# Performance work log

Hardware: AMD Instinct MI355X
Metric: run time of the kernel (lower is better)

## Reference

```python
import jax, jax.numpy as jnp
import numpy as np

N = 16384          # points in the (single-batch) cloud
K = 16             # boundary_k
C = 20             # num semantic classes (ScanNet-style)
IGNORE = -1        # ignore_index
BOUNDARY_W = 1.0   # boundary_loss_weight


def setup_inputs() -> dict:
    key = jax.random.key(0)
    k1, k2, k3 = jax.random.split(key, 3)
    coord = jax.random.normal(k1, (N, 3), jnp.float32)
    seg_logits = jax.random.normal(k2, (N, C), jnp.float32)
    segment = jax.random.randint(k3, (N,), 0, C, dtype=jnp.int32)
    return {"coord": coord, "seg_logits": seg_logits, "segment": segment, "offset": N}


def _knn_idx(coord):
    # brute-force kNN (loop=False): exclude self via +inf diagonal
    d2 = jnp.sum(coord * coord, axis=1)                       # [N]
    dist = d2[:, None] + d2[None, :] - 2.0 * (coord @ coord.T)  # [N, N]
    dist = dist + jnp.where(jnp.eye(dist.shape[0], dtype=bool), jnp.inf, 0.0)
    _, idx = jax.lax.top_k(-dist, K)                          # [N, K] neighbor (src) indices per center (dst)
    return idx


def _masked_ce(logp_tgt, mask):
    # mean cross-entropy over masked points (matches torch reduction='mean' w/ ignore_index)
    cnt = jnp.sum(mask)
    s = jnp.sum(jnp.where(mask, logp_tgt, 0.0))
    return jnp.where(cnt > 0, -s / jnp.maximum(cnt, 1).astype(logp_tgt.dtype), 0.0)


def reference(coord, seg_logits, segment, offset):
    # --- boundary mask: knn_graph -> per-edge label diff -> scatter-max to dst ---
    nbr = _knn_idx(coord)                                     # [N, K] src indices, dst = row index
    nbr_seg = segment[nbr]                                    # gather: [N, K]
    valid_pt = segment != IGNORE                              # [N]
    valid = (nbr_seg != IGNORE) & valid_pt[:, None]           # per-edge valid
    diff = valid & (nbr_seg != segment[:, None])              # per-edge label mismatch
    boundary = jnp.any(diff, axis=1)                          # scatter-max over dst == row-wise any

    # --- main loss: cross-entropy with ignore_index ---
    logp = jax.nn.log_softmax(seg_logits, axis=-1)            # [N, C]
    tgt = jnp.clip(segment, 0, C - 1)
    logp_tgt = jnp.take_along_axis(logp, tgt[:, None], axis=1)[:, 0]  # [N]
    main_loss = _masked_ce(logp_tgt, valid_pt)

    # --- boundary loss: CE restricted to boundary points (0 if none) ---
    bmask = boundary & valid_pt
    boundary_loss = _masked_ce(logp_tgt, bmask)

    loss = main_loss + BOUNDARY_W * boundary_loss
    return loss
```

## Files before the change

kernel.cpp:

```cpp
#include <hip/hip_runtime.h>
#include <hip/hip_bf16.h>
#include <math.h>

#define N_PTS 16384
#define KNN   16
#define NCLS  20
#define BND_W 1.0f

#define THREADS 512
#define WAVES   8
#define FR      4
#define RPW     (16 * FR)
#define RPB     (WAVES * RPW)
#define RBLKS   (N_PTS / RPB)
#define CPB     512
#define CSPLIT  (N_PTS / CPB)

typedef short  short8 __attribute__((ext_vector_type(8)));
typedef float  f32x4  __attribute__((ext_vector_type(4)));

__device__ __forceinline__ unsigned enc_f(float f) {
    unsigned b = __float_as_uint(f);
    return (b & 0x80000000u) ? ~b : (b | 0x80000000u);
}
__device__ __forceinline__ float dec_f(unsigned u) {
    unsigned b = (u & 0x80000000u) ? (u ^ 0x80000000u) : ~u;
    return __uint_as_float(b);
}

__device__ __forceinline__ unsigned short f2bf(float x) {
    union { __hip_bfloat16 h; unsigned short u; } cv;
    cv.h = __float2bfloat16(x);
    return cv.u;
}
__device__ __forceinline__ float bf2f(unsigned short b) {
    union { __hip_bfloat16 h; unsigned short u; } cv;
    cv.u = b;
    return __bfloat162float(cv.h);
}

__device__ __forceinline__ void build_b(const float* __restrict__ coord,
                                        const int* __restrict__ seg, int j,
                                        unsigned short* out) {
    float x = coord[3 * j], y = coord[3 * j + 1], z = coord[3 * j + 2];
    int lab = seg[j];
    unsigned short xh = f2bf(x), yh = f2bf(y), zh = f2bf(z);
    unsigned short xl = f2bf(x - bf2f(xh));
    unsigned short yl = f2bf(y - bf2f(yh));
    unsigned short zl = f2bf(z - bf2f(zh));
    float h = 0.5f * fmaf(x, x, fmaf(y, y, z * z));
    unsigned short hh = f2bf(h);
    unsigned short hl = f2bf(h - bf2f(hh));
    out[0] = xh; out[1] = xh; out[2] = xl;
    out[3] = yh; out[4] = yh; out[5] = yl;
    out[6] = zh; out[7] = zh; out[8] = zl;
    out[9]  = hh ^ 0x8000u;
    out[10] = hl ^ 0x8000u;
#pragma unroll
    for (int s = 0; s < NCLS; s++) out[11 + s] = (lab == s) ? 0x3F80u : 0u;
    out[31] = (lab < 0) ? 0x3F80u : 0u;
}

template<bool PASS1>
__device__ __forceinline__ void build_a(const float* __restrict__ coord,
                                        const int* __restrict__ seg, int i,
                                        unsigned short* out) {
    float x = coord[3 * i], y = coord[3 * i + 1], z = coord[3 * i + 2];
    int lab = seg[i];
    unsigned short xh = f2bf(x), yh = f2bf(y), zh = f2bf(z);
    unsigned short xl = f2bf(x - bf2f(xh));
    unsigned short yl = f2bf(y - bf2f(yh));
    unsigned short zl = f2bf(z - bf2f(zh));
    out[0] = xh; out[1] = xl; out[2] = xh;
    out[3] = yh; out[4] = yl; out[5] = yh;
    out[6] = zh; out[7] = zl; out[8] = zh;
    out[9] = 0x3F80u; out[10] = 0x3F80u;
    const unsigned short nb = 0xC480u;
#pragma unroll
    for (int s = 0; s < NCLS; s++) out[11 + s] = (PASS1 && lab == s) ? nb : 0u;
    out[31] = PASS1 ? nb : 0u;
}

__global__ __launch_bounds__(256) void k_init(unsigned* __restrict__ smax_enc,
                                              int* __restrict__ cnt,
                                              float* __restrict__ accum,
                                              unsigned* __restrict__ done) {
    int i = blockIdx.x * 256 + threadIdx.x;
    smax_enc[i] = enc_f(-3.0e38f);
    cnt[i] = 0;
    if (i < 4) accum[i] = 0.f;
    if (i == 4) *done = 0u;
}

template<bool PASS1>
__global__ __launch_bounds__(THREADS) void k_pass(const float* __restrict__ coord,
                                                  const int* __restrict__ seg,
                                                  unsigned* __restrict__ smax_enc,
                                                  int* __restrict__ cnt) {
    __shared__ __align__(16) unsigned short smem[CPB * 32];
    const int tid  = threadIdx.x;
    const int lane = tid & 63, wave = tid >> 6;
    const int l15  = lane & 15, l4 = lane >> 4;
    const int rb   = blockIdx.x * RPB;
    const int cb   = blockIdx.y * CPB;

    float thr[FR][4];
    int   cv[FR][4];
    f32x4 rmax[FR];
    if (PASS1) {
#pragma unroll
        for (int f = 0; f < FR; f++)
#pragma unroll
            for (int r = 0; r < 4; r++) rmax[f][r] = -3.0e38f;
    } else {
#pragma unroll
        for (int f = 0; f < FR; f++) {
            int row0 = rb + wave * RPW + f * 16 + l4 * 4;
#pragma unroll
            for (int r = 0; r < 4; r++) {
                thr[f][r] = dec_f(smax_enc[row0 + r]);
                cv[f][r] = 0;
            }
        }
    }

    build_a<PASS1>(coord, seg, rb + tid, &smem[tid * 32]);
    __syncthreads();
    short8 af[FR];
    {
        const short8* ap = (const short8*)smem;
#pragma unroll
        for (int f = 0; f < FR; f++)
            af[f] = ap[(wave * RPW + f * 16 + l15) * 4 + l4];
    }
    __syncthreads();

    {
        __attribute__((aligned(16))) unsigned short be[32];
        build_b(coord, seg, cb + tid, be);
        short8* wp = (short8*)smem;
        int swz = (tid >> 1) & 3;
#pragma unroll
        for (int kb = 0; kb < 4; kb++)
            wp[tid * 4 + (kb ^ swz)] = ((const short8*)be)[kb];
    }
    __syncthreads();

    const short8* bp = (const short8*)smem;
    const int bidx = l15 * 4 + (l4 ^ ((l15 >> 1) & 3));
    const f32x4 zero = {0.f, 0.f, 0.f, 0.f};

#pragma unroll 2
    for (int c0 = 0; c0 < CPB; c0 += 32) {
        short8 bA = bp[bidx + c0 * 4];
        short8 bB = bp[bidx + (c0 + 16) * 4];
        f32x4 dA[FR], dB[FR];
#pragma unroll
        for (int f = 0; f < FR; f++)
            dA[f] = __builtin_amdgcn_mfma_f32_16x16x32_bf16(af[f], bA, zero, 0, 0, 0);
#pragma unroll
        for (int f = 0; f < FR; f++)
            dB[f] = __builtin_amdgcn_mfma_f32_16x16x32_bf16(af[f], bB, zero, 0, 0, 0);
        if (PASS1) {
#pragma unroll
            for (int f = 0; f < FR; f++)
#pragma unroll
                for (int r = 0; r < 4; r++)
                    rmax[f][r] = fmaxf(fmaxf(rmax[f][r], dA[f][r]), dB[f][r]);
        } else {
#pragma unroll
            for (int f = 0; f < FR; f++)
#pragma unroll
                for (int r = 0; r < 4; r++)
                    cv[f][r] += ((dA[f][r] > thr[f][r]) ? 1 : 0)
                              + ((dB[f][r] > thr[f][r]) ? 1 : 0);
        }
    }

    if (PASS1) {
#pragma unroll
        for (int m = 1; m < 16; m <<= 1)
#pragma unroll
            for (int f = 0; f < FR; f++)
#pragma unroll
                for (int r = 0; r < 4; r++)
                    rmax[f][r] = fmaxf(rmax[f][r], __shfl_xor(rmax[f][r], m, 64));
        if (l15 == 0) {
#pragma unroll
            for (int f = 0; f < FR; f++) {
                int row0 = rb + wave * RPW + f * 16 + l4 * 4;
#pragma unroll
                for (int r = 0; r < 4; r++)
                    atomicMax(&smax_enc[row0 + r], enc_f(rmax[f][r]));
            }
        }
    } else {
#pragma unroll
        for (int m = 1; m < 16; m <<= 1)
#pragma unroll
            for (int f = 0; f < FR; f++)
#pragma unroll
                for (int r = 0; r < 4; r++)
                    cv[f][r] += __shfl_xor(cv[f][r], m, 64);
        if (l15 == 0) {
#pragma unroll
            for (int f = 0; f < FR; f++) {
                int row0 = rb + wave * RPW + f * 16 + l4 * 4;
#pragma unroll
                for (int r = 0; r < 4; r++)
                    atomicAdd(&cnt[row0 + r], cv[f][r]);
            }
        }
    }
}

__device__ __forceinline__ float waveReduceSum(float v) {
#pragma unroll
    for (int off = 32; off > 0; off >>= 1) v += __shfl_down(v, off, 64);
    return v;
}

__global__ __launch_bounds__(256) void k_ce(const float* __restrict__ logits,
                                            const int* __restrict__ seg,
                                            const int* __restrict__ cnt,
                                            float* __restrict__ accum,
                                            unsigned* __restrict__ done,
                                            float* __restrict__ out) {
    const int i = blockIdx.x * 256 + threadIdx.x;
    float s_main = 0.f, n_main = 0.f, s_bnd = 0.f, n_bnd = 0.f;
    {
        int s = seg[i];
        bool valid = (s != -1);
        const float4* row4 = (const float4*)(logits + (size_t)i * NCLS);
        float a[NCLS];
        float4 v0 = row4[0], v1 = row4[1], v2 = row4[2], v3 = row4[3], v4 = row4[4];
        a[0]=v0.x; a[1]=v0.y; a[2]=v0.z; a[3]=v0.w;
        a[4]=v1.x; a[5]=v1.y; a[6]=v1.z; a[7]=v1.w;
        a[8]=v2.x; a[9]=v2.y; a[10]=v2.z; a[11]=v2.w;
        a[12]=v3.x; a[13]=v3.y; a[14]=v3.z; a[15]=v3.w;
        a[16]=v4.x; a[17]=v4.y; a[18]=v4.z; a[19]=v4.w;
        float m = a[0];
#pragma unroll
        for (int c = 1; c < NCLS; c++) m = fmaxf(m, a[c]);
        float se = 0.f;
#pragma unroll
        for (int c = 0; c < NCLS; c++) se += __expf(a[c] - m);
        int tgt = min(max(s, 0), NCLS - 1);
        float at = 0.f;
#pragma unroll
        for (int c = 0; c < NCLS; c++) at += (c == tgt) ? a[c] : 0.f;
        float logp = at - m - __logf(se);
        bool bnd = valid && ((cnt[i] - 1) < KNN);
        if (valid) { s_main = logp; n_main = 1.f; }
        if (bnd)   { s_bnd  = logp; n_bnd  = 1.f; }
    }
    s_main = waveReduceSum(s_main);
    n_main = waveReduceSum(n_main);
    s_bnd  = waveReduceSum(s_bnd);
    n_bnd  = waveReduceSum(n_bnd);
    if ((threadIdx.x & 63) == 0) {
        atomicAdd(&accum[0], s_main);
        atomicAdd(&accum[1], n_main);
        atomicAdd(&accum[2], s_bnd);
        atomicAdd(&accum[3], n_bnd);
    }
    __syncthreads();
    if (threadIdx.x == 0) {
        __threadfence();
        unsigned old = atomicAdd(done, 1u);
        if (old == gridDim.x - 1) {
            float sm = atomicAdd(&accum[0], 0.f);
            float cm = atomicAdd(&accum[1], 0.f);
            float sb = atomicAdd(&accum[2], 0.f);
            float cb = atomicAdd(&accum[3], 0.f);
            float main_loss = (cm > 0.f) ? (-sm / fmaxf(cm, 1.f)) : 0.f;
            float bnd_loss  = (cb > 0.f) ? (-sb / fmaxf(cb, 1.f)) : 0.f;
            out[0] = main_loss + BND_W * bnd_loss;
        }
    }
}

extern "C" void kernel_launch(void* const* d_in, const int* in_sizes, int n_in,
                              void* d_out, int out_size, void* d_ws, size_t ws_size,
                              hipStream_t stream) {
    const float* coord  = (const float*)d_in[0];
    const float* logits = (const float*)d_in[1];
    const int*   seg    = (const int*)d_in[2];
    (void)in_sizes; (void)n_in; (void)out_size; (void)ws_size;

    unsigned* smax_enc = (unsigned*)d_ws;
    int*      cnt      = (int*)((char*)d_ws + N_PTS * 4);
    float*    accum    = (float*)((char*)d_ws + 2 * N_PTS * 4);
    unsigned* done     = (unsigned*)((char*)d_ws + 2 * N_PTS * 4 + 16);

    dim3 grid(RBLKS, CSPLIT);
    k_init       <<<N_PTS / 256, 256, 0, stream>>>(smax_enc, cnt, accum, done);
    k_pass<true> <<<grid, THREADS, 0, stream>>>(coord, seg, smax_enc, cnt);
    k_pass<false><<<grid, THREADS, 0, stream>>>(coord, seg, smax_enc, cnt);
    k_ce         <<<N_PTS / 256, 256, 0, stream>>>(logits, seg, cnt, accum, done, (float*)d_out);
}
```

Baseline: 71.98 us.

## Replace atomics with per-split partial buffers and loop over candidate chunks

Each block now handles 256 rows against 1024 candidates, looping over two LDS chunks of 512, with 16 column splits instead of 32. The global atomicMax/atomicAdd reductions are replaced by plain writes into per-split partial arrays, which pass 2 and the CE kernel reduce. This removes the init kernel and the atomic contention. The cost is smaller per-wave row tiles (2 fragments instead of 4, so less B-operand reuse) and extra partial reads in the consumer kernels.

```diff
diff --git a/kernel.cpp b/kernel.cpp
--- a/kernel.cpp
+++ b/kernel.cpp
@@ -9,24 +9,16 @@
 
 #define THREADS 512
 #define WAVES   8
-#define FR      4
-#define RPW     (16 * FR)
+#define RPW     32
 #define RPB     (WAVES * RPW)
 #define RBLKS   (N_PTS / RPB)
-#define CPB     512
-#define CSPLIT  (N_PTS / CPB)
+#define CSPLIT  16
+#define CAND_PB (N_PTS / CSPLIT)
+#define CHUNK   512
+#define NCHUNK  (CAND_PB / CHUNK)
 
 typedef short  short8 __attribute__((ext_vector_type(8)));
 typedef float  f32x4  __attribute__((ext_vector_type(4)));
-
-__device__ __forceinline__ unsigned enc_f(float f) {
-    unsigned b = __float_as_uint(f);
-    return (b & 0x80000000u) ? ~b : (b | 0x80000000u);
-}
-__device__ __forceinline__ float dec_f(unsigned u) {
-    unsigned b = (u & 0x80000000u) ? (u ^ 0x80000000u) : ~u;
-    return __uint_as_float(b);
-}
 
 __device__ __forceinline__ unsigned short f2bf(float x) {
     union { __hip_bfloat16 h; unsigned short u; } cv;
@@ -81,134 +73,132 @@
     out[31] = PASS1 ? nb : 0u;
 }
 
-__global__ __launch_bounds__(256) void k_init(unsigned* __restrict__ smax_enc,
-                                              int* __restrict__ cnt,
-                                              float* __restrict__ accum,
-                                              unsigned* __restrict__ done) {
-    int i = blockIdx.x * 256 + threadIdx.x;
-    smax_enc[i] = enc_f(-3.0e38f);
-    cnt[i] = 0;
-    if (i < 4) accum[i] = 0.f;
-    if (i == 4) *done = 0u;
-}
-
 template<bool PASS1>
-__global__ __launch_bounds__(THREADS) void k_pass(const float* __restrict__ coord,
-                                                  const int* __restrict__ seg,
-                                                  unsigned* __restrict__ smax_enc,
-                                                  int* __restrict__ cnt) {
-    __shared__ __align__(16) unsigned short smem[CPB * 32];
+__global__ __launch_bounds__(THREADS, 6) void k_pass(const float* __restrict__ coord,
+                                                     const int* __restrict__ seg,
+                                                     float* __restrict__ smax_part,
+                                                     int* __restrict__ cnt_part,
+                                                     float* __restrict__ accum,
+                                                     unsigned* __restrict__ done) {
+    __shared__ __align__(16) unsigned short smem[CHUNK * 32];
+    __shared__ float thr_lds[RPB];
     const int tid  = threadIdx.x;
     const int lane = tid & 63, wave = tid >> 6;
     const int l15  = lane & 15, l4 = lane >> 4;
     const int rb   = blockIdx.x * RPB;
-    const int cb   = blockIdx.y * CPB;
-
-    float thr[FR][4];
-    int   cv[FR][4];
-    f32x4 rmax[FR];
-    if (PASS1) {
-#pragma unroll
-        for (int f = 0; f < FR; f++)
-#pragma unroll
-            for (int r = 0; r < 4; r++) rmax[f][r] = -3.0e38f;
-    } else {
-#pragma unroll
-        for (int f = 0; f < FR; f++) {
-            int row0 = rb + wave * RPW + f * 16 + l4 * 4;
-#pragma unroll
-            for (int r = 0; r < 4; r++) {
-                thr[f][r] = dec_f(smax_enc[row0 + r]);
-                cv[f][r] = 0;
-            }
-        }
-    }
-
-    build_a<PASS1>(coord, seg, rb + tid, &smem[tid * 32]);
+    const int split = blockIdx.y;
+    const int cb   = split * CAND_PB;
+
+    if (PASS1 && blockIdx.x == 0 && split == 0 && tid == 0) {
+        accum[0] = 0.f; accum[1] = 0.f; accum[2] = 0.f; accum[3] = 0.f;
+        *done = 0u;
+    }
+
+    if (!PASS1 && tid < RPB) {
+        int row = rb + tid;
+        float m = smax_part[row];
+#pragma unroll
+        for (int s = 1; s < CSPLIT; s++) m = fmaxf(m, smax_part[s * N_PTS + row]);
+        thr_lds[tid] = m;
+    }
+
+    if (tid < RPB) build_a<PASS1>(coord, seg, rb + tid, &smem[tid * 32]);
     __syncthreads();
-    short8 af[FR];
+    short8 af0, af1;
     {
         const short8* ap = (const short8*)smem;
-#pragma unroll
-        for (int f = 0; f < FR; f++)
-            af[f] = ap[(wave * RPW + f * 16 + l15) * 4 + l4];
+        int r0 = wave * RPW + l15;
+        af0 = ap[r0 * 4 + l4];
+        af1 = ap[(r0 + 16) * 4 + l4];
+    }
+    float thr0[4], thr1[4];
+    if (!PASS1) {
+#pragma unroll
+        for (int r = 0; r < 4; r++) {
+            thr0[r] = thr_lds[wave * RPW + l4 * 4 + r];
+            thr1[r] = thr_lds[wave * RPW + 16 + l4 * 4 + r];
+        }
     }
     __syncthreads();
 
-    {
-        __attribute__((aligned(16))) unsigned short be[32];
-        build_b(coord, seg, cb + tid, be);
-        short8* wp = (short8*)smem;
-        int swz = (tid >> 1) & 3;
-#pragma unroll
-        for (int kb = 0; kb < 4; kb++)
-            wp[tid * 4 + (kb ^ swz)] = ((const short8*)be)[kb];
-    }
-    __syncthreads();
+    f32x4 rmax0, rmax1;
+    int cv0[4], cv1[4];
+#pragma unroll
+    for (int r = 0; r < 4; r++) {
+        rmax0[r] = -3.0e38f; rmax1[r] = -3.0e38f;
+        cv0[r] = 0; cv1[r] = 0;
+    }
 
     const short8* bp = (const short8*)smem;
     const int bidx = l15 * 4 + (l4 ^ ((l15 >> 1) & 3));
     const f32x4 zero = {0.f, 0.f, 0.f, 0.f};
 
-#pragma unroll 2
-    for (int c0 = 0; c0 < CPB; c0 += 32) {
-        short8 bA = bp[bidx + c0 * 4];
-        short8 bB = bp[bidx + (c0 + 16) * 4];
-        f32x4 dA[FR], dB[FR];
-#pragma unroll
-        for (int f = 0; f < FR; f++)
-            dA[f] = __builtin_amdgcn_mfma_f32_16x16x32_bf16(af[f], bA, zero, 0, 0, 0);
-#pragma unroll
-        for (int f = 0; f < FR; f++)
-            dB[f] = __builtin_amdgcn_mfma_f32_16x16x32_bf16(af[f], bB, zero, 0, 0, 0);
-        if (PASS1) {
-#pragma unroll
-            for (int f = 0; f < FR; f++)
-#pragma unroll
-                for (int r = 0; r < 4; r++)
-                    rmax[f][r] = fmaxf(fmaxf(rmax[f][r], dA[f][r]), dB[f][r]);
-        } else {
-#pragma unroll
-            for (int f = 0; f < FR; f++)
-#pragma unroll
-                for (int r = 0; r < 4; r++)
-                    cv[f][r] += ((dA[f][r] > thr[f][r]) ? 1 : 0)
-                              + ((dB[f][r] > thr[f][r]) ? 1 : 0);
-        }
-    }
-
+    for (int cc = 0; cc < NCHUNK; cc++) {
+        {
+            __attribute__((aligned(16))) unsigned short be[32];
+            build_b(coord, seg, cb + cc * CHUNK + tid, be);
+            short8* wp = (short8*)smem;
+            int swz = (tid >> 1) & 3;
+#pragma unroll
+            for (int kb = 0; kb < 4; kb++)
+                wp[tid * 4 + (kb ^ swz)] = ((const short8*)be)[kb];
+        }
+        __syncthreads();
+
+#pragma unroll 4
+        for (int c0 = 0; c0 < CHUNK; c0 += 32) {
+            short8 bA = bp[bidx + c0 * 4];
+            short8 bB = bp[bidx + (c0 + 16) * 4];
+            f32x4 dA0 = __builtin_amdgcn_mfma_f32_16x16x32_bf16(af0, bA, zero, 0, 0, 0);
+            f32x4 dA1 = __builtin_amdgcn_mfma_f32_16x16x32_bf16(af1, bA, zero, 0, 0, 0);
+            f32x4 dB0 = __builtin_amdgcn_mfma_f32_16x16x32_bf16(af0, bB, zero, 0, 0, 0);
+            f32x4 dB1 = __builtin_amdgcn_mfma_f32_16x16x32_bf16(af1, bB, zero, 0, 0, 0);
+            if (PASS1) {
+#pragma unroll
+                for (int r = 0; r < 4; r++) {
+                    rmax0[r] = fmaxf(fmaxf(rmax0[r], dA0[r]), dB0[r]);
+                    rmax1[r] = fmaxf(fmaxf(rmax1[r], dA1[r]), dB1[r]);
+                }
+            } else {
+#pragma unroll
+                for (int r = 0; r < 4; r++) {
+                    cv0[r] += ((dA0[r] > thr0[r]) ? 1 : 0) + ((dB0[r] > thr0[r]) ? 1 : 0);
+                    cv1[r] += ((dA1[r] > thr1[r]) ? 1 : 0) + ((dB1[r] > thr1[r]) ? 1 : 0);
+                }
+            }
+        }
+        __syncthreads();
+    }
+
+    const int row0 = rb + wave * RPW + l4 * 4;
     if (PASS1) {
 #pragma unroll
         for (int m = 1; m < 16; m <<= 1)
 #pragma unroll
-            for (int f = 0; f < FR; f++)
-#pragma unroll
-                for (int r = 0; r < 4; r++)
-                    rmax[f][r] = fmaxf(rmax[f][r], __shfl_xor(rmax[f][r], m, 64));
+            for (int r = 0; r < 4; r++) {
+                rmax0[r] = fmaxf(rmax0[r], __shfl_xor(rmax0[r], m, 64));
+                rmax1[r] = fmaxf(rmax1[r], __shfl_xor(rmax1[r], m, 64));
+            }
         if (l15 == 0) {
 #pragma unroll
-            for (int f = 0; f < FR; f++) {
-                int row0 = rb + wave * RPW + f * 16 + l4 * 4;
-#pragma unroll
-                for (int r = 0; r < 4; r++)
-                    atomicMax(&smax_enc[row0 + r], enc_f(rmax[f][r]));
+            for (int r = 0; r < 4; r++) {
+                smax_part[split * N_PTS + row0 + r]      = rmax0[r];
+                smax_part[split * N_PTS + row0 + 16 + r] = rmax1[r];
             }
         }
     } else {
 #pragma unroll
         for (int m = 1; m < 16; m <<= 1)
 #pragma unroll
-            for (int f = 0; f < FR; f++)
-#pragma unroll
-                for (int r = 0; r < 4; r++)
-                    cv[f][r] += __shfl_xor(cv[f][r], m, 64);
+            for (int r = 0; r < 4; r++) {
+                cv0[r] += __shfl_xor(cv0[r], m, 64);
+                cv1[r] += __shfl_xor(cv1[r], m, 64);
+            }
         if (l15 == 0) {
 #pragma unroll
-            for (int f = 0; f < FR; f++) {
-                int row0 = rb + wave * RPW + f * 16 + l4 * 4;
-#pragma unroll
-                for (int r = 0; r < 4; r++)
-                    atomicAdd(&cnt[row0 + r], cv[f][r]);
+            for (int r = 0; r < 4; r++) {
+                cnt_part[split * N_PTS + row0 + r]      = cv0[r];
+                cnt_part[split * N_PTS + row0 + 16 + r] = cv1[r];
             }
         }
     }
@@ -222,7 +212,7 @@
 
 __global__ __launch_bounds__(256) void k_ce(const float* __restrict__ logits,
                                             const int* __restrict__ seg,
-                                            const int* __restrict__ cnt,
+                                            const int* __restrict__ cnt_part,
                                             float* __restrict__ accum,
                                             unsigned* __restrict__ done,
                                             float* __restrict__ out) {
@@ -250,7 +240,10 @@
 #pragma unroll
         for (int c = 0; c < NCLS; c++) at += (c == tgt) ? a[c] : 0.f;
         float logp = at - m - __logf(se);
-        bool bnd = valid && ((cnt[i] - 1) < KNN);
+        int cnt = 0;
+#pragma unroll
+        for (int sp = 0; sp < CSPLIT; sp++) cnt += cnt_part[sp * N_PTS + i];
+        bool bnd = valid && ((cnt - 1) < KNN);
         if (valid) { s_main = logp; n_main = 1.f; }
         if (bnd)   { s_bnd  = logp; n_bnd  = 1.f; }
     }
@@ -288,14 +281,13 @@
     const int*   seg    = (const int*)d_in[2];
     (void)in_sizes; (void)n_in; (void)out_size; (void)ws_size;
 
-    unsigned* smax_enc = (unsigned*)d_ws;
-    int*      cnt      = (int*)((char*)d_ws + N_PTS * 4);
-    float*    accum    = (float*)((char*)d_ws + 2 * N_PTS * 4);
-    unsigned* done     = (unsigned*)((char*)d_ws + 2 * N_PTS * 4 + 16);
+    float*    smax_part = (float*)d_ws;
+    int*      cnt_part  = (int*)((char*)d_ws + CSPLIT * N_PTS * 4);
+    float*    accum     = (float*)((char*)d_ws + 2 * CSPLIT * N_PTS * 4);
+    unsigned* done      = (unsigned*)((char*)d_ws + 2 * CSPLIT * N_PTS * 4 + 16);
 
     dim3 grid(RBLKS, CSPLIT);
-    k_init       <<<N_PTS / 256, 256, 0, stream>>>(smax_enc, cnt, accum, done);
-    k_pass<true> <<<grid, THREADS, 0, stream>>>(coord, seg, smax_enc, cnt);
-    k_pass<false><<<grid, THREADS, 0, stream>>>(coord, seg, smax_enc, cnt);
-    k_ce         <<<N_PTS / 256, 256, 0, stream>>>(logits, seg, cnt, accum, done, (float*)d_out);
-}
+    k_pass<true> <<<grid, THREADS, 0, stream>>>(coord, seg, smax_part, cnt_part, accum, done);
+    k_pass<false><<<grid, THREADS, 0, stream>>>(coord, seg, smax_part, cnt_part, accum, done);
+    k_ce         <<<N_PTS / 256, 256, 0, stream>>>(logits, seg, cnt_part, accum, done, (float*)d_out);
+}
```

New measurement: 64.33 us. 1.12x faster.

## Fuse init and CE into kNN passes, split-partial row max without atomics

Applied to the files above, without the earlier changes.

Removes the init and cross-entropy kernels. Init now runs inside pass 1, and the CE reduction runs in the last pass-2 block per row group, detected with a per-row-block done counter. Pass 1 writes per-split partial row maxima instead of encoded atomicMax, and pass 2 reduces those partials into a shared threshold array. The column split grows from 32 to 16 splits of 1024 candidates, A fragments are built directly in registers, and launch bounds now request occupancy 4. This cuts launch count and atomics, but pass 2 grows 16 extra loads per row and serialises the CE work at the tail.

```diff
diff --git a/kernel.cpp b/kernel.cpp
--- a/kernel.cpp
+++ b/kernel.cpp
@@ -13,20 +13,11 @@
 #define RPW     (16 * FR)
 #define RPB     (WAVES * RPW)
 #define RBLKS   (N_PTS / RPB)
-#define CPB     512
-#define CSPLIT  (N_PTS / CPB)
+#define CSPLIT  16
+#define CAND_PB (N_PTS / CSPLIT)
 
 typedef short  short8 __attribute__((ext_vector_type(8)));
 typedef float  f32x4  __attribute__((ext_vector_type(4)));
-
-__device__ __forceinline__ unsigned enc_f(float f) {
-    unsigned b = __float_as_uint(f);
-    return (b & 0x80000000u) ? ~b : (b | 0x80000000u);
-}
-__device__ __forceinline__ float dec_f(unsigned u) {
-    unsigned b = (u & 0x80000000u) ? (u ^ 0x80000000u) : ~u;
-    return __uint_as_float(b);
-}
 
 __device__ __forceinline__ unsigned short f2bf(float x) {
     union { __hip_bfloat16 h; unsigned short u; } cv;
@@ -62,96 +53,124 @@
 }
 
 template<bool PASS1>
-__device__ __forceinline__ void build_a(const float* __restrict__ coord,
-                                        const int* __restrict__ seg, int i,
-                                        unsigned short* out) {
-    float x = coord[3 * i], y = coord[3 * i + 1], z = coord[3 * i + 2];
-    int lab = seg[i];
-    unsigned short xh = f2bf(x), yh = f2bf(y), zh = f2bf(z);
-    unsigned short xl = f2bf(x - bf2f(xh));
-    unsigned short yl = f2bf(y - bf2f(yh));
-    unsigned short zl = f2bf(z - bf2f(zh));
-    out[0] = xh; out[1] = xl; out[2] = xh;
-    out[3] = yh; out[4] = yl; out[5] = yh;
-    out[6] = zh; out[7] = zl; out[8] = zh;
-    out[9] = 0x3F80u; out[10] = 0x3F80u;
-    const unsigned short nb = 0xC480u;
-#pragma unroll
-    for (int s = 0; s < NCLS; s++) out[11 + s] = (PASS1 && lab == s) ? nb : 0u;
-    out[31] = PASS1 ? nb : 0u;
-}
-
-__global__ __launch_bounds__(256) void k_init(unsigned* __restrict__ smax_enc,
-                                              int* __restrict__ cnt,
-                                              float* __restrict__ accum,
-                                              unsigned* __restrict__ done) {
-    int i = blockIdx.x * 256 + threadIdx.x;
-    smax_enc[i] = enc_f(-3.0e38f);
-    cnt[i] = 0;
-    if (i < 4) accum[i] = 0.f;
-    if (i == 4) *done = 0u;
+__device__ __forceinline__ short8 build_a_frag(const float* __restrict__ coord,
+                                               const int* __restrict__ seg,
+                                               int row, int g) {
+    __attribute__((aligned(16))) unsigned short s[8];
+    const unsigned short one = 0x3F80u;
+    const unsigned short nb = PASS1 ? 0xC480u : 0u;
+    if (g == 0) {
+        float x = coord[3 * row], y = coord[3 * row + 1], z = coord[3 * row + 2];
+        unsigned short xh = f2bf(x), yh = f2bf(y), zh = f2bf(z);
+        s[0] = xh; s[1] = f2bf(x - bf2f(xh)); s[2] = xh;
+        s[3] = yh; s[4] = f2bf(y - bf2f(yh)); s[5] = yh;
+        s[6] = zh; s[7] = f2bf(z - bf2f(zh));
+    } else if (g == 1) {
+        float z = coord[3 * row + 2];
+        int lab = seg[row];
+        s[0] = f2bf(z); s[1] = one; s[2] = one;
+        s[3] = (lab == 0) ? nb : 0u; s[4] = (lab == 1) ? nb : 0u;
+        s[5] = (lab == 2) ? nb : 0u; s[6] = (lab == 3) ? nb : 0u;
+        s[7] = (lab == 4) ? nb : 0u;
+    } else if (g == 2) {
+        int lab = seg[row];
+        s[0] = (lab == 5) ? nb : 0u;  s[1] = (lab == 6) ? nb : 0u;
+        s[2] = (lab == 7) ? nb : 0u;  s[3] = (lab == 8) ? nb : 0u;
+        s[4] = (lab == 9) ? nb : 0u;  s[5] = (lab == 10) ? nb : 0u;
+        s[6] = (lab == 11) ? nb : 0u; s[7] = (lab == 12) ? nb : 0u;
+    } else {
+        int lab = seg[row];
+        s[0] = (lab == 13) ? nb : 0u; s[1] = (lab == 14) ? nb : 0u;
+        s[2] = (lab == 15) ? nb : 0u; s[3] = (lab == 16) ? nb : 0u;
+        s[4] = (lab == 17) ? nb : 0u; s[5] = (lab == 18) ? nb : 0u;
+        s[6] = (lab == 19) ? nb : 0u; s[7] = nb;
+    }
+    return *(const short8*)s;
+}
+
+__device__ __forceinline__ float waveReduceSum(float v) {
+#pragma unroll
+    for (int off = 32; off > 0; off >>= 1) v += __shfl_down(v, off, 64);
+    return v;
 }
 
 template<bool PASS1>
-__global__ __launch_bounds__(THREADS) void k_pass(const float* __restrict__ coord,
-                                                  const int* __restrict__ seg,
-                                                  unsigned* __restrict__ smax_enc,
-                                                  int* __restrict__ cnt) {
-    __shared__ __align__(16) unsigned short smem[CPB * 32];
+__global__ __launch_bounds__(THREADS, 4) void k_pass(
+    const float* __restrict__ coord, const int* __restrict__ seg,
+    const float* __restrict__ logits,
+    float* __restrict__ smax_part, int* __restrict__ cnt,
+    float* __restrict__ accum, int* __restrict__ done_rb,
+    unsigned* __restrict__ done_final, float* __restrict__ out)
+{
+    __shared__ __align__(16) unsigned short bsm[CAND_PB * 32];
+    __shared__ float thr_lds[RPB];
+    __shared__ int s_flag;
     const int tid  = threadIdx.x;
     const int lane = tid & 63, wave = tid >> 6;
     const int l15  = lane & 15, l4 = lane >> 4;
     const int rb   = blockIdx.x * RPB;
-    const int cb   = blockIdx.y * CPB;
-
-    float thr[FR][4];
-    int   cv[FR][4];
-    f32x4 rmax[FR];
-    if (PASS1) {
-#pragma unroll
-        for (int f = 0; f < FR; f++)
-#pragma unroll
-            for (int r = 0; r < 4; r++) rmax[f][r] = -3.0e38f;
-    } else {
-#pragma unroll
-        for (int f = 0; f < FR; f++) {
-            int row0 = rb + wave * RPW + f * 16 + l4 * 4;
-#pragma unroll
-            for (int r = 0; r < 4; r++) {
-                thr[f][r] = dec_f(smax_enc[row0 + r]);
-                cv[f][r] = 0;
-            }
-        }
-    }
-
-    build_a<PASS1>(coord, seg, rb + tid, &smem[tid * 32]);
-    __syncthreads();
-    short8 af[FR];
-    {
-        const short8* ap = (const short8*)smem;
-#pragma unroll
-        for (int f = 0; f < FR; f++)
-            af[f] = ap[(wave * RPW + f * 16 + l15) * 4 + l4];
-    }
-    __syncthreads();
+    const int split = blockIdx.y;
+    const int cb   = split * CAND_PB;
+
+    if (PASS1 && split == 0) {
+        cnt[rb + tid] = 0;
+        if (tid == 5) done_rb[blockIdx.x] = 0;
+        if (blockIdx.x == 0) {
+            if (tid < 4) accum[tid] = 0.f;
+            if (tid == 4) *done_final = 0u;
+        }
+    }
 
     {
         __attribute__((aligned(16))) unsigned short be[32];
-        build_b(coord, seg, cb + tid, be);
-        short8* wp = (short8*)smem;
-        int swz = (tid >> 1) & 3;
-#pragma unroll
-        for (int kb = 0; kb < 4; kb++)
-            wp[tid * 4 + (kb ^ swz)] = ((const short8*)be)[kb];
+        short8* wp = (short8*)bsm;
+#pragma unroll
+        for (int u = 0; u < 2; u++) {
+            int c = 2 * tid + u;
+            build_b(coord, seg, cb + c, be);
+            int swz = (c >> 1) & 3;
+#pragma unroll
+            for (int kb = 0; kb < 4; kb++)
+                wp[c * 4 + (kb ^ swz)] = ((const short8*)be)[kb];
+        }
+    }
+
+    short8 af[FR];
+#pragma unroll
+    for (int f = 0; f < FR; f++)
+        af[f] = build_a_frag<PASS1>(coord, seg, rb + wave * RPW + f * 16 + l15, l4);
+
+    if (!PASS1) {
+        int row = rb + tid;
+        float m = smax_part[row];
+#pragma unroll
+        for (int s = 1; s < CSPLIT; s++) m = fmaxf(m, smax_part[s * N_PTS + row]);
+        thr_lds[tid] = m;
     }
     __syncthreads();
 
-    const short8* bp = (const short8*)smem;
+    float thr[FR][4];
+    if (!PASS1) {
+#pragma unroll
+        for (int f = 0; f < FR; f++)
+#pragma unroll
+            for (int r = 0; r < 4; r++)
+                thr[f][r] = thr_lds[wave * RPW + f * 16 + l4 * 4 + r];
+    }
+
+    f32x4 rmax[FR];
+    int cv[FR][4];
+#pragma unroll
+    for (int f = 0; f < FR; f++)
+#pragma unroll
+        for (int r = 0; r < 4; r++) { rmax[f][r] = -3.0e38f; cv[f][r] = 0; }
+
+    const short8* bp = (const short8*)bsm;
     const int bidx = l15 * 4 + (l4 ^ ((l15 >> 1) & 3));
     const f32x4 zero = {0.f, 0.f, 0.f, 0.f};
 
 #pragma unroll 2
-    for (int c0 = 0; c0 < CPB; c0 += 32) {
+    for (int c0 = 0; c0 < CAND_PB; c0 += 32) {
         short8 bA = bp[bidx + c0 * 4];
         short8 bB = bp[bidx + (c0 + 16) * 4];
         f32x4 dA[FR], dB[FR];
@@ -187,12 +206,10 @@
                     rmax[f][r] = fmaxf(rmax[f][r], __shfl_xor(rmax[f][r], m, 64));
         if (l15 == 0) {
 #pragma unroll
-            for (int f = 0; f < FR; f++) {
-                int row0 = rb + wave * RPW + f * 16 + l4 * 4;
-#pragma unroll
-                for (int r = 0; r < 4; r++)
-                    atomicMax(&smax_enc[row0 + r], enc_f(rmax[f][r]));
-            }
+            for (int f = 0; f < FR; f++)
+#pragma unroll
+                for (int r = 0; r < 4; r++)
+                    smax_part[split * N_PTS + rb + wave * RPW + f * 16 + l4 * 4 + r] = rmax[f][r];
         }
     } else {
 #pragma unroll
@@ -204,78 +221,66 @@
                     cv[f][r] += __shfl_xor(cv[f][r], m, 64);
         if (l15 == 0) {
 #pragma unroll
-            for (int f = 0; f < FR; f++) {
-                int row0 = rb + wave * RPW + f * 16 + l4 * 4;
-#pragma unroll
-                for (int r = 0; r < 4; r++)
-                    atomicAdd(&cnt[row0 + r], cv[f][r]);
+            for (int f = 0; f < FR; f++)
+#pragma unroll
+                for (int r = 0; r < 4; r++)
+                    atomicAdd(&cnt[rb + wave * RPW + f * 16 + l4 * 4 + r], cv[f][r]);
+        }
+
+        __syncthreads();
+        if (tid == 0) {
+            __threadfence();
+            s_flag = (atomicAdd(&done_rb[blockIdx.x], 1) == CSPLIT - 1) ? 1 : 0;
+        }
+        __syncthreads();
+        if (s_flag) {
+            const int row = rb + tid;
+            int sg = seg[row];
+            bool valid = (sg != -1);
+            const float4* row4 = (const float4*)(logits + (size_t)row * NCLS);
+            float a[NCLS];
+            float4 v0 = row4[0], v1 = row4[1], v2 = row4[2], v3 = row4[3], v4 = row4[4];
+            a[0]=v0.x; a[1]=v0.y; a[2]=v0.z; a[3]=v0.w;
+            a[4]=v1.x; a[5]=v1.y; a[6]=v1.z; a[7]=v1.w;
+            a[8]=v2.x; a[9]=v2.y; a[10]=v2.z; a[11]=v2.w;
+            a[12]=v3.x; a[13]=v3.y; a[14]=v3.z; a[15]=v3.w;
+            a[16]=v4.x; a[17]=v4.y; a[18]=v4.z; a[19]=v4.w;
+            float mx = a[0];
+#pragma unroll
+            for (int c = 1; c < NCLS; c++) mx = fmaxf(mx, a[c]);
+            float se = 0.f;
+#pragma unroll
+            for (int c = 0; c < NCLS; c++) se += __expf(a[c] - mx);
+            int tgt = min(max(sg, 0), NCLS - 1);
+            float at = 0.f;
+#pragma unroll
+            for (int c = 0; c < NCLS; c++) at += (c == tgt) ? a[c] : 0.f;
+            float logp = at - mx - __logf(se);
+            int crow = atomicAdd(&cnt[row], 0);
+            bool bnd = valid && ((crow - 1) < KNN);
+            float sm = valid ? logp : 0.f, nm = valid ? 1.f : 0.f;
+            float sb = bnd ? logp : 0.f,  nb2 = bnd ? 1.f : 0.f;
+            sm = waveReduceSum(sm); nm = waveReduceSum(nm);
+            sb = waveReduceSum(sb); nb2 = waveReduceSum(nb2);
+            if ((tid & 63) == 0) {
+                atomicAdd(&accum[0], sm);
+                atomicAdd(&accum[1], nm);
+                atomicAdd(&accum[2], sb);
+                atomicAdd(&accum[3], nb2);
             }
-        }
-    }
-}
-
-__device__ __forceinline__ float waveReduceSum(float v) {
-#pragma unroll
-    for (int off = 32; off > 0; off >>= 1) v += __shfl_down(v, off, 64);
-    return v;
-}
-
-__global__ __launch_bounds__(256) void k_ce(const float* __restrict__ logits,
-                                            const int* __restrict__ seg,
-                                            const int* __restrict__ cnt,
-                                            float* __restrict__ accum,
-                                            unsigned* __restrict__ done,
-                                            float* __restrict__ out) {
-    const int i = blockIdx.x * 256 + threadIdx.x;
-    float s_main = 0.f, n_main = 0.f, s_bnd = 0.f, n_bnd = 0.f;
-    {
-        int s = seg[i];
-        bool valid = (s != -1);
-        const float4* row4 = (const float4*)(logits + (size_t)i * NCLS);
-        float a[NCLS];
-        float4 v0 = row4[0], v1 = row4[1], v2 = row4[2], v3 = row4[3], v4 = row4[4];
-        a[0]=v0.x; a[1]=v0.y; a[2]=v0.z; a[3]=v0.w;
-        a[4]=v1.x; a[5]=v1.y; a[6]=v1.z; a[7]=v1.w;
-        a[8]=v2.x; a[9]=v2.y; a[10]=v2.z; a[11]=v2.w;
-        a[12]=v3.x; a[13]=v3.y; a[14]=v3.z; a[15]=v3.w;
-        a[16]=v4.x; a[17]=v4.y; a[18]=v4.z; a[19]=v4.w;
-        float m = a[0];
-#pragma unroll
-        for (int c = 1; c < NCLS; c++) m = fmaxf(m, a[c]);
-        float se = 0.f;
-#pragma unroll
-        for (int c = 0; c < NCLS; c++) se += __expf(a[c] - m);
-        int tgt = min(max(s, 0), NCLS - 1);
-        float at = 0.f;
-#pragma unroll
-        for (int c = 0; c < NCLS; c++) at += (c == tgt) ? a[c] : 0.f;
-        float logp = at - m - __logf(se);
-        bool bnd = valid && ((cnt[i] - 1) < KNN);
-        if (valid) { s_main = logp; n_main = 1.f; }
-        if (bnd)   { s_bnd  = logp; n_bnd  = 1.f; }
-    }
-    s_main = waveReduceSum(s_main);
-    n_main = waveReduceSum(n_main);
-    s_bnd  = waveReduceSum(s_bnd);
-    n_bnd  = waveReduceSum(n_bnd);
-    if ((threadIdx.x & 63) == 0) {
-        atomicAdd(&accum[0], s_main);
-        atomicAdd(&accum[1], n_main);
-        atomicAdd(&accum[2], s_bnd);
-        atomicAdd(&accum[3], n_bnd);
-    }
-    __syncthreads();
-    if (threadIdx.x == 0) {
-        __threadfence();
-        unsigned old = atomicAdd(done, 1u);
-        if (old == gridDim.x - 1) {
-            float sm = atomicAdd(&accum[0], 0.f);
-            float cm = atomicAdd(&accum[1], 0.f);
-            float sb = atomicAdd(&accum[2], 0.f);
-            float cb = atomicAdd(&accum[3], 0.f);
-            float main_loss = (cm > 0.f) ? (-sm / fmaxf(cm, 1.f)) : 0.f;
-            float bnd_loss  = (cb > 0.f) ? (-sb / fmaxf(cb, 1.f)) : 0.f;
-            out[0] = main_loss + BND_W * bnd_loss;
+            __syncthreads();
+            if (tid == 0) {
+                __threadfence();
+                if (atomicAdd(done_final, 1u) == (unsigned)(RBLKS - 1)) {
+                    float Sm = atomicAdd(&accum[0], 0.f);
+                    float Cm = atomicAdd(&accum[1], 0.f);
+                    float Sb = atomicAdd(&accum[2], 0.f);
+                    float Cb = atomicAdd(&accum[3], 0.f);
+                    float main_loss = (Cm > 0.f) ? (-Sm / fmaxf(Cm, 1.f)) : 0.f;
+                    float bnd_loss  = (Cb > 0.f) ? (-Sb / fmaxf(Cb, 1.f)) : 0.f;
+                    out[0] = main_loss + BND_W * bnd_loss;
+                }
+            }
         }
     }
 }
@@ -288,14 +293,16 @@
     const int*   seg    = (const int*)d_in[2];
     (void)in_sizes; (void)n_in; (void)out_size; (void)ws_size;
 
-    unsigned* smax_enc = (unsigned*)d_ws;
-    int*      cnt      = (int*)((char*)d_ws + N_PTS * 4);
-    float*    accum    = (float*)((char*)d_ws + 2 * N_PTS * 4);
-    unsigned* done     = (unsigned*)((char*)d_ws + 2 * N_PTS * 4 + 16);
+    float*    smax_part = (float*)d_ws;
+    int*      cnt       = (int*)((char*)d_ws + CSPLIT * N_PTS * 4);
+    char*     tail      = (char*)d_ws + CSPLIT * N_PTS * 4 + N_PTS * 4;
+    float*    accum     = (float*)tail;
+    int*      done_rb   = (int*)(tail + 16);
+    unsigned* done_final= (unsigned*)(tail + 16 + RBLKS * 4);
 
     dim3 grid(RBLKS, CSPLIT);
-    k_init       <<<N_PTS / 256, 256, 0, stream>>>(smax_enc, cnt, accum, done);
-    k_pass<true> <<<grid, THREADS, 0, stream>>>(coord, seg, smax_enc, cnt);
-    k_pass<false><<<grid, THREADS, 0, stream>>>(coord, seg, smax_enc, cnt);
-    k_ce         <<<N_PTS / 256, 256, 0, stream>>>(logits, seg, cnt, accum, done, (float*)d_out);
-}
+    k_pass<true> <<<grid, THREADS, 0, stream>>>(coord, seg, logits, smax_part, cnt,
+                                                accum, done_rb, done_final, (float*)d_out);
+    k_pass<false><<<grid, THREADS, 0, stream>>>(coord, seg, logits, smax_part, cnt,
+                                                accum, done_rb, done_final, (float*)d_out);
+}
```

Result: faster. 64.02 us (-11.1%).
